# Kernel tuning notes

Hardware: AMD Instinct MI355X
Metric: run time of the kernel (lower is better)

Reference implementation:

```python
import jax, jax.numpy as jnp
import numpy as np
import math

RAND_N = 32
B = 262144
MAX_DEG = 9
P = MAX_DEG + 1  # padded Legendre polynomial length
EPS = 1e-8


def _rot_xyz(a, b, c):
    # scipy Rotation.from_euler('xyz', [a,b,c]) (extrinsic): R = Rz(c) @ Ry(b) @ Rx(a)
    ca, sa = math.cos(a), math.sin(a)
    cb, sb = math.cos(b), math.sin(b)
    cc, sc = math.cos(c), math.sin(c)
    Rx = np.array([[1, 0, 0], [0, ca, -sa], [0, sa, ca]])
    Ry = np.array([[cb, 0, sb], [0, 1, 0], [-sb, 0, cb]])
    Rz = np.array([[cc, -sc, 0], [sc, cc, 0], [0, 0, 1]])
    return Rz @ Ry @ Rx


def setup_inputs() -> dict:
    key = jax.random.key(0)
    k1, k2 = jax.random.split(key)
    rng = np.random.default_rng(0)

    # random rotation matrices (buffer 'matrices')
    angs = rng.random((RAND_N, 3)) * 2.0 * np.pi
    matrices = np.stack([_rot_xyz(*a) for a in angs]).astype(np.float32)

    # degrees ~ N(0,10) clipped to [1,9], int (buffer 'degrees')
    degs = np.clip(rng.normal(0.0, 10.0, (RAND_N,)), 1, 9).astype(np.int32)

    # per-basis Legendre coeffs (increasing power, zero-padded) + scalar constants
    coeffs_pad = np.zeros((RAND_N, P), np.float32)
    coeff_scale = np.zeros((RAND_N,), np.float32)
    y0_norm = np.zeros((RAND_N,), np.float32)
    for i, l in enumerate(degs):
        l = int(l)
        c = np.polynomial.legendre.leg2poly(np.eye(l + 1)[l])  # == scipy legendre(l).c[::-1]
        coeffs_pad[i, : l + 1] = c
        logc = -2 * math.log(l) - math.lgamma(l + 1) + 0.5 * (math.lgamma(2 * l + 2) - math.log(4 * math.pi))
        coeff_scale[i] = ((-1) ** l) * math.exp(logc)
        y0_norm[i] = math.sqrt((2 * l + 1) / (4 * math.pi))

    vec = jax.random.normal(k1, (B, 3), jnp.float32)
    vec = vec / jnp.linalg.norm(vec, axis=-1, keepdims=True)  # unit directions
    roughness = jax.random.uniform(k2, (B, 1), jnp.float32, 0.01, 1.0)

    return {
        "vec": vec,
        "roughness": roughness,
        "matrices": jnp.asarray(matrices),
        "coeffs_pad": jnp.asarray(coeffs_pad),
        "coeff_scale": jnp.asarray(coeff_scale),
        "y0_norm": jnp.asarray(y0_norm),
        "degrees": jnp.asarray(degs),
    }


def reference(vec, roughness, matrices, coeffs_pad, coeff_scale, y0_norm, degrees):
    # vec: (B,3), roughness: (B,1)
    kappa = 1.0 / (roughness + EPS)                          # (B,1)
    rvec = jnp.einsum('bi,nij->bnj', vec, matrices)          # (B,N,3) all bases at once
    x_, y_, z_ = rvec[..., 0], rvec[..., 1], rvec[..., 2]
    phi = jnp.arctan2(y_, x_)                                # (B,N)
    theta = jnp.arctan2(z_, jnp.sqrt(x_ * x_ + y_ * y_)) - jnp.pi / 2

    # ragged-degree Legendre power series, padded to P terms
    ct = jnp.cos(theta)                                      # (B,N)
    powers = jnp.arange(P)                                   # (P,) int exponents
    v = jnp.einsum('bnp,np->bn', ct[..., None] ** powers, coeffs_pad)
    y0 = y0_norm * v                                         # (B,N)

    # real part of coeff * sin(theta)^deg * exp(i*deg*phi)  (deg>=1 so ind=1 branch)
    yl1 = coeff_scale * (jnp.sin(theta) ** degrees) * jnp.cos(degrees * phi)

    # Al(l, kappa) = exp(-l(l+1)/2/(kappa+eps)); broadcasts (B,1)x(N,) -> (B,N)
    al = jnp.exp(-(degrees * (degrees + 1)).astype(jnp.float32) * 0.5 / (kappa + EPS))

    out = al[..., None] * jnp.stack([y0, yl1], axis=-1)      # (B,N,2)
    return out.reshape(out.shape[0], -1)                     # (B, 2*N)
```

## Files before the change

kernel.cpp:

```cpp
#include <hip/hip_runtime.h>
#include <math.h>


#define NBASIS 32
#define PLEN 10
#define EPSV 1e-8f
#define LOG2E 1.44269504088896340736f
#define ROWD 65
#define NT 2

typedef float f32x4 __attribute__((ext_vector_type(4)));

__global__ __launch_bounds__(256) void randish_kernel(
    const float* __restrict__ vec,
    const float* __restrict__ rough,
    const float* __restrict__ mats,
    const float* __restrict__ coeffs,
    const float* __restrict__ cscale,
    const float* __restrict__ y0n,
    const int*   __restrict__ degs,
    float* __restrict__ out,
    int B)
{
    __shared__ float lds[64 * ROWD];

    const int t    = threadIdx.x;
    const int lane = t & 63;
    const int w    = t >> 6;

    float V0[NT], V1[NT], V2[NT], TC[NT];
    int   BB[NT];
#pragma unroll
    for (int it = 0; it < NT; ++it) {
        const int b0 = (blockIdx.x * NT + it) * 64;
        const int b  = b0 + lane;
        BB[it] = b0;
        V0[it] = vec[b * 3 + 0];
        V1[it] = vec[b * 3 + 1];
        V2[it] = vec[b * 3 + 2];
        TC[it] = (rough[b] + EPSV) * (-0.5f * LOG2E);
    }

    float* row = &lds[lane * ROWD];

#pragma unroll
    for (int it = 0; it < NT; ++it) {
        const float v0 = V0[it], v1 = V1[it], v2 = V2[it], tc = TC[it];

#pragma unroll
        for (int j = 0; j < 8; ++j) {
            const int n = __builtin_amdgcn_readfirstlane(8 * w + j);
            const int d = __builtin_amdgcn_readfirstlane(degs[n]);
            const int par = d & 1;

            const float xh = fmaf(v0, mats[n*9+0], fmaf(v1, mats[n*9+3], v2 * mats[n*9+6]));
            const float yh = fmaf(v0, mats[n*9+1], fmaf(v1, mats[n*9+4], v2 * mats[n*9+7]));
            const float ct = fmaf(v0, mats[n*9+2], fmaf(v1, mats[n*9+5], v2 * mats[n*9+8]));

            const float ct2 = ct * ct;
            float v = coeffs[n*PLEN + par + 8];
            v = fmaf(v, ct2, coeffs[n*PLEN + par + 6]);
            v = fmaf(v, ct2, coeffs[n*PLEN + par + 4]);
            v = fmaf(v, ct2, coeffs[n*PLEN + par + 2]);
            v = fmaf(v, ct2, coeffs[n*PLEN + par + 0]);
            if (par) v *= ct;

            float R = xh;
            if (d > 1) {
                const float ss  = fmaf(yh, yh, xh * xh);
                const float m2x = xh + xh;
                float Rm2 = 1.0f, Rm1 = xh;
                for (int k = 2; k <= d; ++k) {
                    const float Rk = fmaf(m2x, Rm1, -(ss * Rm2));
                    Rm2 = Rm1;
                    Rm1 = Rk;
                }
                R = Rm1;
            }
            float cs = cscale[n];
            if (par) cs = -cs;

            const float al = __builtin_amdgcn_exp2f((float)(d * (d + 1)) * tc);

            row[2 * n + 0] = al * (y0n[n] * v);
            row[2 * n + 1] = al * (cs * R);
        }

        __syncthreads();

        f32x4* outp = reinterpret_cast<f32x4*>(out + (size_t)BB[it] * 64);
#pragma unroll
        for (int p = 0; p < 4; ++p) {
            const int c  = p * 256 + t;
            const int r  = c >> 4;
            const int c4 = (c & 15) * 4;
            const float* src = &lds[r * ROWD + c4];
            f32x4 o = { src[0], src[1], src[2], src[3] };
            __builtin_nontemporal_store(o, outp + c);
        }

        if (it + 1 < NT) __syncthreads();
    }
}

extern "C" void kernel_launch(void* const* d_in, const int* in_sizes, int n_in,
                              void* d_out, int out_size, void* d_ws, size_t ws_size,
                              hipStream_t stream) {
    const float* vec    = (const float*)d_in[0];
    const float* rough  = (const float*)d_in[1];
    const float* mats   = (const float*)d_in[2];
    const float* coeffs = (const float*)d_in[3];
    const float* cscale = (const float*)d_in[4];
    const float* y0n    = (const float*)d_in[5];
    const int*   degs   = (const int*)d_in[6];
    float* out = (float*)d_out;

    const int B = in_sizes[1];
    const int block = 256;
    const int grid = B / (64 * NT);

    randish_kernel<<<grid, block, 0, stream>>>(vec, rough, mats, coeffs, cscale,
                                               y0n, degs, out, B);
}
```

Measured before the change: 20.49 us.

## Double-buffer LDS tiles with 512-thread blocks to overlap compute and stores

Doubles the block to 512 threads, so each wave now computes 4 bases per row instead of 8, and each block handles 4 row tiles instead of 2. Two LDS buffers let the next tile be computed while the current tile's transposed output is streamed out, which removes one barrier per tile. The aim is to hide global store latency behind computation and expose more parallelism per block. In exchange it uses twice the LDS and produces half as many blocks, which may lower occupancy or leave CUs imbalanced.

Measured after the change: 21.67 us. 5.8% more time.

```diff
diff --git a/kernel.cpp b/kernel.cpp
--- a/kernel.cpp
+++ b/kernel.cpp
@@ -7,11 +7,11 @@
 #define EPSV 1e-8f
 #define LOG2E 1.44269504088896340736f
 #define ROWD 65
-#define NT 2
+#define NTILE 4
 
 typedef float f32x4 __attribute__((ext_vector_type(4)));
 
-__global__ __launch_bounds__(256) void randish_kernel(
+__global__ __launch_bounds__(512) void randish_kernel(
     const float* __restrict__ vec,
     const float* __restrict__ rough,
     const float* __restrict__ mats,
@@ -22,17 +22,17 @@
     float* __restrict__ out,
     int B)
 {
-    __shared__ float lds[64 * ROWD];
+    __shared__ float lds[2][64 * ROWD];
 
     const int t    = threadIdx.x;
     const int lane = t & 63;
     const int w    = t >> 6;
 
-    float V0[NT], V1[NT], V2[NT], TC[NT];
-    int   BB[NT];
+    float V0[NTILE], V1[NTILE], V2[NTILE], TC[NTILE];
+    int   BB[NTILE];
 #pragma unroll
-    for (int it = 0; it < NT; ++it) {
-        const int b0 = (blockIdx.x * NT + it) * 64;
+    for (int it = 0; it < NTILE; ++it) {
+        const int b0 = (blockIdx.x * NTILE + it) * 64;
         const int b  = b0 + lane;
         BB[it] = b0;
         V0[it] = vec[b * 3 + 0];
@@ -41,15 +41,12 @@
         TC[it] = (rough[b] + EPSV) * (-0.5f * LOG2E);
     }
 
-    float* row = &lds[lane * ROWD];
-
+    auto compute_tile = [&](int it, int buf) {
+        const float v0 = V0[it], v1 = V1[it], v2 = V2[it], tc = TC[it];
+        float* row = &lds[buf][lane * ROWD];
 #pragma unroll
-    for (int it = 0; it < NT; ++it) {
-        const float v0 = V0[it], v1 = V1[it], v2 = V2[it], tc = TC[it];
-
-#pragma unroll
-        for (int j = 0; j < 8; ++j) {
-            const int n = __builtin_amdgcn_readfirstlane(8 * w + j);
+        for (int j = 0; j < 4; ++j) {
+            const int n = __builtin_amdgcn_readfirstlane(4 * w + j);
             const int d = __builtin_amdgcn_readfirstlane(degs[n]);
             const int par = d & 1;
 
@@ -85,21 +82,30 @@
             row[2 * n + 0] = al * (y0n[n] * v);
             row[2 * n + 1] = al * (cs * R);
         }
+    };
 
-        __syncthreads();
-
+    auto store_tile = [&](int it, int buf) {
         f32x4* outp = reinterpret_cast<f32x4*>(out + (size_t)BB[it] * 64);
 #pragma unroll
-        for (int p = 0; p < 4; ++p) {
-            const int c  = p * 256 + t;
+        for (int p = 0; p < 2; ++p) {
+            const int c  = p * 512 + t;
             const int r  = c >> 4;
             const int c4 = (c & 15) * 4;
-            const float* src = &lds[r * ROWD + c4];
+            const float* src = &lds[buf][r * ROWD + c4];
             f32x4 o = { src[0], src[1], src[2], src[3] };
             __builtin_nontemporal_store(o, outp + c);
         }
+    };
 
-        if (it + 1 < NT) __syncthreads();
+    compute_tile(0, 0);
+    __syncthreads();
+#pragma unroll
+    for (int it = 0; it < NTILE; ++it) {
+        store_tile(it, it & 1);
+        if (it + 1 < NTILE) {
+            compute_tile(it + 1, (it + 1) & 1);
+            __syncthreads();
+        }
     }
 }
 
@@ -116,8 +122,8 @@
     float* out = (float*)d_out;
 
     const int B = in_sizes[1];
-    const int block = 256;
-    const int grid = B / (64 * NT);
+    const int block = 512;
+    const int grid = B / (64 * NTILE);
 
     randish_kernel<<<grid, block, 0, stream>>>(vec, rough, mats, coeffs, cscale,
                                                y0n, degs, out, B);
```
